# Kernel optimization log

Measured on AMD Instinct MI355X. Metric: run time of the kernel, lower is better.

## Reference

```python
import jax, jax.numpy as jnp
import numpy as np

B = 4096
N_QUBITS = 4
N_LAYERS = 3
C64 = jnp.complex64


def setup_inputs() -> dict:
    key = jax.random.key(0)
    ks = jax.random.split(key, 14)
    f = jax.random.normal
    return {
        "x": f(ks[0], (B, 1, 28, 28), jnp.float32),
        "qparams": f(ks[1], (N_LAYERS, N_QUBITS, 3), jnp.float32),
        "dw4_w": f(ks[2], (4, 1, 4, 4), jnp.float32) * 0.1,
        "dw4_b": f(ks[3], (4,), jnp.float32) * 0.1,
        "pw4_w": f(ks[4], (4, 4, 1, 1), jnp.float32) * 0.3,
        "pw4_b": f(ks[5], (4,), jnp.float32) * 0.1,
        "dw8_w": f(ks[6], (4, 1, 8, 8), jnp.float32) * 0.05,
        "dw8_b": f(ks[7], (4,), jnp.float32) * 0.1,
        "pw8_w": f(ks[8], (4, 4, 1, 1), jnp.float32) * 0.3,
        "pw8_b": f(ks[9], (4,), jnp.float32) * 0.1,
        "res_w": f(ks[10], (4, 1, 1, 1), jnp.float32) * 0.3,
        "res_b": f(ks[11], (4,), jnp.float32) * 0.1,
        "head_w": f(ks[12], (10, 4 * 3 * 14 * 14), jnp.float32) * 0.02,
        "head_b": f(ks[13], (10,), jnp.float32) * 0.02,
    }


def _rx(t):
    c = jnp.cos(t / 2).astype(C64)
    s = (-1j * jnp.sin(t / 2)).astype(C64)
    return jnp.stack([jnp.stack([c, s]), jnp.stack([s, c])])


def _ry(t):
    c = jnp.cos(t / 2)
    s = jnp.sin(t / 2)
    return jnp.stack([jnp.stack([c, -s]), jnp.stack([s, c])]).astype(C64)


def _rz(t):
    z = jnp.zeros((), C64)
    return jnp.stack([jnp.stack([jnp.exp(-0.5j * t).astype(C64), z]),
                      jnp.stack([z, jnp.exp(0.5j * t).astype(C64)])])


def _apply_1q(state, U, wire):
    # state: (n,2,2,2,2); U: (2,2) shared across patches
    st = jnp.moveaxis(state, wire + 1, -1)
    st = jnp.einsum('ij,n...j->n...i', U, st)
    return jnp.moveaxis(st, -1, wire + 1)


def _apply_1q_batched(state, U, wire):
    # U: (n,2,2), one gate per patch (input encoding)
    st = jnp.moveaxis(state, wire + 1, -1)
    st = jnp.einsum('nij,n...j->n...i', U, st)
    return jnp.moveaxis(st, -1, wire + 1)


def _cnot(state, c, t):
    a, b = jnp.split(state, 2, axis=c + 1)
    return jnp.concatenate([a, jnp.flip(b, axis=t + 1)], axis=c + 1)


def _quantum_features(patches, params):
    # patches: (n,4) angles; returns (n,4) PauliZ expectations
    n = patches.shape[0]
    state = jnp.zeros((n, 16), C64).at[:, 0].set(1.0).reshape(n, 2, 2, 2, 2)
    c = jnp.cos(patches / 2)
    s = jnp.sin(patches / 2)
    for q in range(N_QUBITS):
        Uq = jnp.stack([jnp.stack([c[:, q], -s[:, q]], -1),
                        jnp.stack([s[:, q], c[:, q]], -1)], -2).astype(C64)
        state = _apply_1q_batched(state, Uq, q)
    for l in range(N_LAYERS):
        for q in range(N_QUBITS):
            state = _apply_1q(state, _rx(params[l, q, 0]), q)
            state = _apply_1q(state, _ry(params[l, q, 1]), q)
            state = _apply_1q(state, _rz(params[l, q, 2]), q)
        for q in range(N_QUBITS - 1):
            state = _cnot(state, q, q + 1)
        state = _cnot(state, N_QUBITS - 1, 0)
    probs = jnp.real(state * jnp.conj(state))  # (n,2,2,2,2)
    ez = [jnp.sum(jnp.take(probs, 0, axis=q + 1) - jnp.take(probs, 1, axis=q + 1),
                  axis=(1, 2, 3)) for q in range(N_QUBITS)]
    return jnp.stack(ez, -1).astype(jnp.float32)


def _conv(x, w, b, stride):
    y = jax.lax.conv_general_dilated(x, w, (stride, stride), 'VALID',
                                     dimension_numbers=('NCHW', 'OIHW', 'NCHW'))
    return y + b[None, :, None, None]


def _forward(x, qparams, dw4_w, dw4_b, pw4_w, pw4_b, dw8_w, dw8_b, pw8_w, pw8_b,
             res_w, res_b, head_w, head_b):
    b = x.shape[0]
    # residual branch: 1x1 conv then 2x2 avg-pool down to the 14x14 grid
    res = _conv(x, res_w, res_b, 1)                      # (B,4,28,28)
    res = res.reshape(b, 4, 14, 2, 14, 2).mean(axis=(3, 5))  # (B,4,14,14)
    # quantum branch over non-overlapping 2x2 patches
    patches = x[:, 0].reshape(b, 14, 2, 14, 2).transpose(0, 1, 3, 2, 4)
    patches = patches.reshape(b * 14 * 14, 4)
    feat2 = _quantum_features(patches, qparams).reshape(b, 14, 14, 4)
    # multi-scale conv branches, upsampled (nearest) to the 14x14 grid
    feat4 = jax.nn.relu(_conv(_conv(x, dw4_w, dw4_b, 4), pw4_w, pw4_b, 1))  # (B,4,7,7)
    feat4 = jnp.repeat(jnp.repeat(feat4, 2, axis=2), 2, axis=3)             # (B,4,14,14)
    feat8 = jax.nn.relu(_conv(_conv(x, dw8_w, dw8_b, 8), pw8_w, pw8_b, 1))  # (B,4,3,3)
    feat8 = jax.image.resize(feat8, (b, 4, 14, 14), 'nearest')
    f4 = jnp.transpose(feat4, (0, 2, 3, 1))
    f8 = jnp.transpose(feat8, (0, 2, 3, 1))
    r = jnp.transpose(res, (0, 2, 3, 1))
    out = jnp.concatenate([feat2, f4, f8], axis=3) + jnp.tile(r, (1, 1, 1, 3))
    logits = out.reshape(b, -1) @ head_w.T + head_b
    return jax.nn.log_softmax(logits, axis=-1)


def reference(x, qparams, dw4_w, dw4_b, pw4_w, pw4_b, dw8_w, dw8_b, pw8_w, pw8_b,
              res_w, res_b, head_w, head_b):
    return _forward(x, qparams, dw4_w, dw4_b, pw4_w, pw4_b, dw8_w, dw8_b,
                    pw8_w, pw8_b, res_w, res_b, head_w, head_b)
```

## Files before the change

kernel.cpp:

```cpp
#include <hip/hip_runtime.h>

#define WS_T    0
#define WS_HQ   512
#define WS_WA   8352
#define WS_H4   10312
#define WS_H8   12272
#define WS_C10  12632

__device__ __forceinline__ float4 f4fma(const float4 a, const float s, const float4 c) {
  return {fmaf(a.x, s, c.x), fmaf(a.y, s, c.y), fmaf(a.z, s, c.z), fmaf(a.w, s, c.w)};
}
__device__ __forceinline__ float4 f4fma4(const float4 a, const float4 b, const float4 c) {
  return {fmaf(a.x, b.x, c.x), fmaf(a.y, b.y, c.y), fmaf(a.z, b.z, c.z), fmaf(a.w, b.w, c.w)};
}
__device__ __forceinline__ float hsum4(const float4 a) {
  return a.x + a.y + a.z + a.w;
}

__global__ __launch_bounds__(256) void prep_kernel(
    const float* __restrict__ qp, const float* __restrict__ hw,
    const float* __restrict__ res_w, const float* __restrict__ res_b,
    const float* __restrict__ hb, float* __restrict__ ws) {
  __shared__ float row[2352];
  __shared__ float cred[4];
  __shared__ float Sr[16][16];
  __shared__ float Si[16][16];
  __shared__ float csc[36], css[36];
  __shared__ float Afs[256][4];
  const int t = threadIdx.x;

  if (blockIdx.x < 10) {
    const int k = blockIdx.x;
    for (int i = t; i < 2352; i += 256) row[i] = hw[k * 2352 + i];
    __syncthreads();
    float cpart = 0.f;
    if (t < 196) {
      const int b12 = t * 12;
      float4 h = {row[b12], row[b12 + 1], row[b12 + 2], row[b12 + 3]};
      ((float4*)(ws + WS_HQ))[k * 196 + t] = h;
      float wa = 0.f;
#pragma unroll
      for (int c = 0; c < 4; ++c) {
        const float s3 = row[b12 + c] + row[b12 + 4 + c] + row[b12 + 8 + c];
        wa += res_w[c] * s3;
        cpart += res_b[c] * s3;
      }
      ws[WS_WA + k * 196 + t] = wa;
    }
    if (t < 49) {
      const int i4 = t / 7, j4 = t % 7;
      float4 s = {0.f, 0.f, 0.f, 0.f};
#pragma unroll
      for (int di = 0; di < 2; ++di)
#pragma unroll
        for (int dj = 0; dj < 2; ++dj) {
          const int pos = (2 * i4 + di) * 14 + 2 * j4 + dj;
          s.x += row[pos * 12 + 4]; s.y += row[pos * 12 + 5];
          s.z += row[pos * 12 + 6]; s.w += row[pos * 12 + 7];
        }
      ((float4*)(ws + WS_H4))[k * 49 + t] = s;
    }
    if (t < 9) {
      const int i8 = t / 3, j8 = t % 3;
      const int pi0 = (i8 == 0) ? 0 : ((i8 == 1) ? 5 : 9);
      const int pi1 = (i8 == 0) ? 5 : ((i8 == 1) ? 9 : 14);
      const int pj0 = (j8 == 0) ? 0 : ((j8 == 1) ? 5 : 9);
      const int pj1 = (j8 == 0) ? 5 : ((j8 == 1) ? 9 : 14);
      float4 s = {0.f, 0.f, 0.f, 0.f};
      for (int pi = pi0; pi < pi1; ++pi)
        for (int pj = pj0; pj < pj1; ++pj) {
          const int pos = pi * 14 + pj;
          s.x += row[pos * 12 + 8]; s.y += row[pos * 12 + 9];
          s.z += row[pos * 12 + 10]; s.w += row[pos * 12 + 11];
        }
      ((float4*)(ws + WS_H8))[k * 9 + t] = s;
    }
#pragma unroll
    for (int off = 32; off > 0; off >>= 1) cpart += __shfl_xor(cpart, off);
    if ((t & 63) == 0) cred[t >> 6] = cpart;
    __syncthreads();
    if (t == 0) ws[WS_C10 + k] = hb[k] + cred[0] + cred[1] + cred[2] + cred[3];
    return;
  }

  if (t >= 64) return;

  if (t < 36) {
    float th = 0.5f * qp[t];
    csc[t] = cosf(th);
    css[t] = sinf(th);
  }
#pragma unroll
  for (int h = 0; h < 4; ++h) {
    const int idx = t + 64 * h;
    Sr[idx >> 4][idx & 15] = ((idx >> 4) == (idx & 15)) ? 1.f : 0.f;
    Si[idx >> 4][idx & 15] = 0.f;
  }

  for (int l = 0; l < 3; ++l) {
    for (int q = 0; q < 4; ++q) {
      const int m = 8 >> q;
      for (int r = 0; r < 3; ++r) {
        const float c = csc[l * 12 + q * 3 + r];
        const float s = css[l * 12 + q * 3 + r];
#pragma unroll
        for (int h = 0; h < 2; ++h) {
          const int idx = t + 64 * h;
          const int col = idx >> 3, pp = idx & 7;
          const int k = ((pp & ~(m - 1)) << 1) | (pp & (m - 1));
          const int k1 = k | m;
          float a0r = Sr[col][k],  a0i = Si[col][k];
          float a1r = Sr[col][k1], a1i = Si[col][k1];
          float n0r, n0i, n1r, n1i;
          if (r == 0) {
            n0r = c * a0r + s * a1i;  n0i = c * a0i - s * a1r;
            n1r = c * a1r + s * a0i;  n1i = c * a1i - s * a0r;
          } else if (r == 1) {
            n0r = c * a0r - s * a1r;  n0i = c * a0i - s * a1i;
            n1r = s * a0r + c * a1r;  n1i = s * a0i + c * a1i;
          } else {
            n0r = c * a0r + s * a0i;  n0i = c * a0i - s * a0r;
            n1r = c * a1r - s * a1i;  n1i = c * a1i + s * a1r;
          }
          Sr[col][k] = n0r;  Si[col][k] = n0i;
          Sr[col][k1] = n1r; Si[col][k1] = n1i;
        }
      }
    }
    for (int e = 0; e < 4; ++e) {
      const int c2 = t >> 2, p2 = t & 3;
      const int mc = 8 >> e;
      const int mt = 8 >> ((e + 1) & 3);
      const int rest = 15 & ~(mc | mt);
      const int rl = rest & (-rest);
      const int rh = rest ^ rl;
      const int k = mc | ((p2 & 1) ? rl : 0) | ((p2 & 2) ? rh : 0);
      const int k1 = k | mt;
      float tr = Sr[c2][k]; Sr[c2][k] = Sr[c2][k1]; Sr[c2][k1] = tr;
      float ti = Si[c2][k]; Si[c2][k] = Si[c2][k1]; Si[c2][k1] = ti;
    }
  }

#pragma unroll
  for (int h = 0; h < 4; ++h) {
    const int o = t + 64 * h;
    const int i = o >> 4, j = o & 15;
    float a0 = 0.f, a1 = 0.f, a2 = 0.f, a3 = 0.f;
    for (int k = 0; k < 16; ++k) {
      float pr = Sr[i][k] * Sr[j][k] + Si[i][k] * Si[j][k];
      a0 += (k & 8) ? -pr : pr;
      a1 += (k & 4) ? -pr : pr;
      a2 += (k & 2) ? -pr : pr;
      a3 += (k & 1) ? -pr : pr;
    }
    Afs[o][0] = a0; Afs[o][1] = a1; Afs[o][2] = a2; Afs[o][3] = a3;
  }

#pragma unroll
  for (int h = 0; h < 6; ++h) {
    const int o = t + 64 * h;
    if (o < 324) {
      const int mi = o >> 2, q = o & 3;
      const int m0 = mi / 27, m1 = (mi / 9) % 3, m2 = (mi / 3) % 3, m3 = mi % 3;
      const int mm[4] = {m0, m1, m2, m3};
      float acc = 0.f;
      for (int c = 0; c < 16; ++c) {
        int ii = 0, jj = 0; float sg = 1.f;
        for (int qb = 0; qb < 4; ++qb) {
          const int cb = (c >> qb) & 1, bit = 8 >> qb, mq = mm[qb];
          if (mq == 2) { if (cb) ii |= bit; else jj |= bit; }
          else if (cb) { ii |= bit; jj |= bit; if (mq == 1) sg = -sg; }
        }
        acc += sg * Afs[ii * 16 + jj][q];
      }
      ws[WS_T + mi * 4 + q] = acc * 0.0625f;
    }
  }
}

__global__ __launch_bounds__(256, 4) void qmain_kernel(
    const float* __restrict__ x, const float4* __restrict__ T4,
    const float4* __restrict__ HQ4, const float* __restrict__ WA,
    const float4* __restrict__ H44, const float4* __restrict__ H84,
    const float* __restrict__ C10,
    const float* __restrict__ dw4_w, const float* __restrict__ dw4_b,
    const float* __restrict__ pw4_w, const float* __restrict__ pw4_b,
    const float* __restrict__ dw8_w, const float* __restrict__ dw8_b,
    const float* __restrict__ pw8_w, const float* __restrict__ pw8_b,
    float* __restrict__ out, const int B) {
  __shared__ __align__(16) float xs[4 * 792];
  const int t = threadIdx.x;
  const int w = t >> 6, lane = t & 63;
  const int img = blockIdx.x * 4 + w;
  float* xw = xs + w * 792;
  const float4* xw4 = (const float4*)xw;
  const bool ok = (img < B);

  if (ok) {
    const float4* xg = (const float4*)(x + img * 784);
#pragma unroll
    for (int it = 0; it < 4; ++it) {
      const int idx = it * 64 + lane;
      if (idx < 196) ((float4*)xw)[idx] = xg[idx];
    }
  }

  float acc[10];
#pragma unroll
  for (int k = 0; k < 10; ++k) acc[k] = 0.f;

  if (ok && lane < 49) {
    float cc[4][4], ss[4][4], av[4];
#pragma unroll
    for (int s = 0; s < 4; ++s) {
      const int p = 49 * s + lane;
      const int base = 56 * (p / 14) + 2 * (p % 14);
      const float2 a01 = *(const float2*)(xw + base);
      const float2 a23 = *(const float2*)(xw + base + 28);
      __sincosf(a01.x, &ss[s][0], &cc[s][0]);
      __sincosf(a01.y, &ss[s][1], &cc[s][1]);
      __sincosf(a23.x, &ss[s][2], &cc[s][2]);
      __sincosf(a23.y, &ss[s][3], &cc[s][3]);
      av[s] = 0.25f * (a01.x + a01.y + a23.x + a23.y);
    }
    float4 e[4];
#pragma unroll
    for (int s = 0; s < 4; ++s) e[s] = {0.f, 0.f, 0.f, 0.f};
#pragma unroll 1
    for (int g = 0; g < 9; ++g) {
      const float4 t0 = T4[g * 9 + 0], t1 = T4[g * 9 + 1], t2 = T4[g * 9 + 2];
      const float4 t3 = T4[g * 9 + 3], t4 = T4[g * 9 + 4], t5 = T4[g * 9 + 5];
      const float4 t6 = T4[g * 9 + 6], t7 = T4[g * 9 + 7], t8 = T4[g * 9 + 8];
      const int m0 = g / 3, m1 = g % 3;
#pragma unroll
      for (int s = 0; s < 4; ++s) {
        const float c3 = cc[s][3], s3 = ss[s][3];
        const float4 u0 = f4fma(t2, s3, f4fma(t1, c3, t0));
        const float4 u1 = f4fma(t5, s3, f4fma(t4, c3, t3));
        const float4 u2 = f4fma(t8, s3, f4fma(t7, c3, t6));
        const float4 inner = f4fma(u2, ss[s][2], f4fma(u1, cc[s][2], u0));
        const float f0 = (m0 == 0) ? 1.f : ((m0 == 1) ? cc[s][0] : ss[s][0]);
        const float f1 = (m1 == 0) ? 1.f : ((m1 == 1) ? cc[s][1] : ss[s][1]);
        const float wf = (m0 == 0) ? f1 : ((m1 == 0) ? f0 : f0 * f1);
        e[s] = f4fma(inner, wf, e[s]);
      }
    }
#pragma unroll
    for (int k = 0; k < 10; ++k) {
      float a = 0.f;
#pragma unroll
      for (int s = 0; s < 4; ++s) {
        const int p = 49 * s + lane;
        const float4 h = HQ4[k * 196 + p];
        a += fmaf(h.x, e[s].x, fmaf(h.y, e[s].y,
             fmaf(h.z, e[s].z, fmaf(h.w, e[s].w, WA[k * 196 + p] * av[s]))));
      }
      acc[k] = a;
    }
    {
      const int u = lane;
      const int i = u / 7, j = u % 7;
      const float4* w44 = (const float4*)dw4_w;
      float4 q0 = {0.f, 0.f, 0.f, 0.f}, q1 = q0, q2 = q0, q3 = q0;
#pragma unroll
      for (int uu = 0; uu < 4; ++uu) {
        const float4 xa = xw4[(4 * i + uu) * 7 + j];
        q0 = f4fma4(w44[0 + uu], xa, q0);
        q1 = f4fma4(w44[4 + uu], xa, q1);
        q2 = f4fma4(w44[8 + uu], xa, q2);
        q3 = f4fma4(w44[12 + uu], xa, q3);
      }
      const float y0 = hsum4(q0) + dw4_b[0];
      const float y1 = hsum4(q1) + dw4_b[1];
      const float y2 = hsum4(q2) + dw4_b[2];
      const float y3 = hsum4(q3) + dw4_b[3];
      float z[4];
#pragma unroll
      for (int o = 0; o < 4; ++o) {
        float zz = pw4_b[o];
        zz = fmaf(pw4_w[o * 4 + 0], y0, zz);
        zz = fmaf(pw4_w[o * 4 + 1], y1, zz);
        zz = fmaf(pw4_w[o * 4 + 2], y2, zz);
        zz = fmaf(pw4_w[o * 4 + 3], y3, zz);
        z[o] = fmaxf(zz, 0.f);
      }
#pragma unroll
      for (int k = 0; k < 10; ++k) {
        const float4 h = H44[k * 49 + u];
        acc[k] += fmaf(h.x, z[0], fmaf(h.y, z[1], fmaf(h.z, z[2], h.w * z[3])));
      }
    }
  } else if (ok && lane >= 49 && lane < 58) {
    const int pos = lane - 49;
    const int i8 = pos / 3, j8 = pos % 3;
    const float4* w84 = (const float4*)dw8_w;
    float4 e0 = {0.f, 0.f, 0.f, 0.f}, e1 = e0, e2 = e0, e3 = e0;
#pragma unroll
    for (int uu = 0; uu < 8; ++uu) {
      const float4 xa = xw4[(8 * i8 + uu) * 7 + 2 * j8];
      const float4 xb = xw4[(8 * i8 + uu) * 7 + 2 * j8 + 1];
      e0 = f4fma4(w84[0 + uu * 2], xa, e0);
      e0 = f4fma4(w84[1 + uu * 2], xb, e0);
      e1 = f4fma4(w84[16 + uu * 2], xa, e1);
      e1 = f4fma4(w84[17 + uu * 2], xb, e1);
      e2 = f4fma4(w84[32 + uu * 2], xa, e2);
      e2 = f4fma4(w84[33 + uu * 2], xb, e2);
      e3 = f4fma4(w84[48 + uu * 2], xa, e3);
      e3 = f4fma4(w84[49 + uu * 2], xb, e3);
    }
    const float d0 = hsum4(e0) + dw8_b[0];
    const float d1 = hsum4(e1) + dw8_b[1];
    const float d2 = hsum4(e2) + dw8_b[2];
    const float d3 = hsum4(e3) + dw8_b[3];
    float z[4];
#pragma unroll
    for (int o = 0; o < 4; ++o) {
      float zz = pw8_b[o];
      zz = fmaf(pw8_w[o * 4 + 0], d0, zz);
      zz = fmaf(pw8_w[o * 4 + 1], d1, zz);
      zz = fmaf(pw8_w[o * 4 + 2], d2, zz);
      zz = fmaf(pw8_w[o * 4 + 3], d3, zz);
      z[o] = fmaxf(zz, 0.f);
    }
#pragma unroll
    for (int k = 0; k < 10; ++k) {
      const float4 h = H84[k * 9 + pos];
      acc[k] += fmaf(h.x, z[0], fmaf(h.y, z[1], fmaf(h.z, z[2], h.w * z[3])));
    }
  }

  if (!ok) return;

#pragma unroll
  for (int k = 0; k < 10; ++k) {
    float v = acc[k];
    v += __shfl_xor(v, 1);
    v += __shfl_xor(v, 2);
    v += __shfl_xor(v, 4);
    v += __shfl_xor(v, 8);
    v += __shfl_xor(v, 16);
    v += __shfl_xor(v, 32);
    acc[k] = v;
  }

  float lg[10], m = -1e30f;
#pragma unroll
  for (int k = 0; k < 10; ++k) {
    lg[k] = acc[k] + C10[k];
    m = fmaxf(m, lg[k]);
  }
  float se = 0.f;
#pragma unroll
  for (int k = 0; k < 10; ++k) se += __expf(lg[k] - m);
  const float ls = m + __logf(se);
  if (lane < 10) {
    float v = lg[0];
#pragma unroll
    for (int k = 1; k < 10; ++k)
      if (lane == k) v = lg[k];
    out[img * 10 + lane] = v - ls;
  }
}

extern "C" void kernel_launch(void* const* d_in, const int* in_sizes, int n_in,
                              void* d_out, int out_size, void* d_ws, size_t ws_size,
                              hipStream_t stream) {
  const float* x      = (const float*)d_in[0];
  const float* qp     = (const float*)d_in[1];
  const float* dw4_w  = (const float*)d_in[2];
  const float* dw4_b  = (const float*)d_in[3];
  const float* pw4_w  = (const float*)d_in[4];
  const float* pw4_b  = (const float*)d_in[5];
  const float* dw8_w  = (const float*)d_in[6];
  const float* dw8_b  = (const float*)d_in[7];
  const float* pw8_w  = (const float*)d_in[8];
  const float* pw8_b  = (const float*)d_in[9];
  const float* res_w  = (const float*)d_in[10];
  const float* res_b  = (const float*)d_in[11];
  const float* head_w = (const float*)d_in[12];
  const float* head_b = (const float*)d_in[13];
  float* out = (float*)d_out;
  float* ws = (float*)d_ws;
  const int B = in_sizes[0] / 784;

  hipLaunchKernelGGL(prep_kernel, dim3(11), dim3(256), 0, stream,
                     qp, head_w, res_w, res_b, head_b, ws);
  hipLaunchKernelGGL(qmain_kernel, dim3((B + 3) / 4), dim3(256), 0, stream,
                     x, (const float4*)(ws + WS_T),
                     (const float4*)(ws + WS_HQ), ws + WS_WA,
                     (const float4*)(ws + WS_H4), (const float4*)(ws + WS_H8),
                     ws + WS_C10,
                     dw4_w, dw4_b, pw4_w, pw4_b, dw8_w, dw8_b, pw8_w, pw8_b,
                     out, B);
}
```

Before: 33.89 us.

## Split quantum feature evaluation into a separate fully parallel per-patch kernel

Moves the per-patch quantum expectation computation out of the main kernel, where only 49 of 64 lanes worked on 4 patches each, into a new kernel with one thread per patch across all images. The results (4 expectations plus the patch average) go to a global workspace and the main kernel reads them back. This raises parallelism and removes lane idling for the trig-heavy part, at the cost of an extra launch and a round trip through global memory of about 16 MB. It also fuses the three rotation gates per qubit in the prep kernel into one pass over shared memory.

```diff
diff --git a/kernel.cpp b/kernel.cpp
--- a/kernel.cpp
+++ b/kernel.cpp
@@ -6,6 +6,8 @@
 #define WS_H4   10312
 #define WS_H8   12272
 #define WS_C10  12632
+#define WS_E4   262144
+#define WS_AV   3473408
 
 __device__ __forceinline__ float4 f4fma(const float4 a, const float s, const float4 c) {
   return {fmaf(a.x, s, c.x), fmaf(a.y, s, c.y), fmaf(a.z, s, c.z), fmaf(a.w, s, c.w)};
@@ -100,31 +102,25 @@
   for (int l = 0; l < 3; ++l) {
     for (int q = 0; q < 4; ++q) {
       const int m = 8 >> q;
-      for (int r = 0; r < 3; ++r) {
-        const float c = csc[l * 12 + q * 3 + r];
-        const float s = css[l * 12 + q * 3 + r];
-#pragma unroll
-        for (int h = 0; h < 2; ++h) {
-          const int idx = t + 64 * h;
-          const int col = idx >> 3, pp = idx & 7;
-          const int k = ((pp & ~(m - 1)) << 1) | (pp & (m - 1));
-          const int k1 = k | m;
-          float a0r = Sr[col][k],  a0i = Si[col][k];
-          float a1r = Sr[col][k1], a1i = Si[col][k1];
-          float n0r, n0i, n1r, n1i;
-          if (r == 0) {
-            n0r = c * a0r + s * a1i;  n0i = c * a0i - s * a1r;
-            n1r = c * a1r + s * a0i;  n1i = c * a1i - s * a0r;
-          } else if (r == 1) {
-            n0r = c * a0r - s * a1r;  n0i = c * a0i - s * a1i;
-            n1r = s * a0r + c * a1r;  n1i = s * a0i + c * a1i;
-          } else {
-            n0r = c * a0r + s * a0i;  n0i = c * a0i - s * a0r;
-            n1r = c * a1r - s * a1i;  n1i = c * a1i + s * a1r;
-          }
-          Sr[col][k] = n0r;  Si[col][k] = n0i;
-          Sr[col][k1] = n1r; Si[col][k1] = n1i;
-        }
+      const float cx = csc[l * 12 + q * 3 + 0], sx = css[l * 12 + q * 3 + 0];
+      const float cy = csc[l * 12 + q * 3 + 1], sy = css[l * 12 + q * 3 + 1];
+      const float cz = csc[l * 12 + q * 3 + 2], sz = css[l * 12 + q * 3 + 2];
+#pragma unroll
+      for (int h = 0; h < 2; ++h) {
+        const int idx = t + 64 * h;
+        const int col = idx >> 3, pp = idx & 7;
+        const int k = ((pp & ~(m - 1)) << 1) | (pp & (m - 1));
+        const int k1 = k | m;
+        float a0r = Sr[col][k],  a0i = Si[col][k];
+        float a1r = Sr[col][k1], a1i = Si[col][k1];
+        const float x0r = cx * a0r + sx * a1i, x0i = cx * a0i - sx * a1r;
+        const float x1r = cx * a1r + sx * a0i, x1i = cx * a1i - sx * a0r;
+        const float y0r = cy * x0r - sy * x1r, y0i = cy * x0i - sy * x1i;
+        const float y1r = sy * x0r + cy * x1r, y1i = sy * x0i + cy * x1i;
+        a0r = cz * y0r + sz * y0i;  a0i = cz * y0i - sz * y0r;
+        a1r = cz * y1r - sz * y1i;  a1i = cz * y1i + sz * y1r;
+        Sr[col][k] = a0r;  Si[col][k] = a0i;
+        Sr[col][k1] = a1r; Si[col][k1] = a1i;
       }
     }
     for (int e = 0; e < 4; ++e) {
@@ -178,8 +174,41 @@
   }
 }
 
+__global__ __launch_bounds__(256) void qfeat_kernel(
+    const float* __restrict__ x, const float4* __restrict__ T4,
+    float4* __restrict__ e4out, float* __restrict__ avout, const int NP) {
+  const int gp = blockIdx.x * 256 + threadIdx.x;
+  if (gp >= NP) return;
+  const int img = gp / 196, p = gp - img * 196;
+  const int pi = p / 14, pj = p - pi * 14;
+  const float* xb = x + img * 784 + 56 * pi + 2 * pj;
+  const float2 a01 = *(const float2*)(xb);
+  const float2 a23 = *(const float2*)(xb + 28);
+  float c0, s0, c1, s1, c2, s2, c3, s3;
+  __sincosf(a01.x, &s0, &c0);
+  __sincosf(a01.y, &s1, &c1);
+  __sincosf(a23.x, &s2, &c2);
+  __sincosf(a23.y, &s3, &c3);
+  const float w01[9] = {1.f, c1, s1, c0, c0 * c1, c0 * s1, s0, s0 * c1, s0 * s1};
+  float4 e = {0.f, 0.f, 0.f, 0.f};
+#pragma unroll
+  for (int g = 0; g < 9; ++g) {
+    const float4 t0 = T4[g * 9 + 0], t1 = T4[g * 9 + 1], t2 = T4[g * 9 + 2];
+    const float4 t3 = T4[g * 9 + 3], t4 = T4[g * 9 + 4], t5 = T4[g * 9 + 5];
+    const float4 t6 = T4[g * 9 + 6], t7 = T4[g * 9 + 7], t8 = T4[g * 9 + 8];
+    const float4 u0 = f4fma(t2, s3, f4fma(t1, c3, t0));
+    const float4 u1 = f4fma(t5, s3, f4fma(t4, c3, t3));
+    const float4 u2 = f4fma(t8, s3, f4fma(t7, c3, t6));
+    const float4 inner = f4fma(u2, s2, f4fma(u1, c2, u0));
+    e = f4fma(inner, w01[g], e);
+  }
+  e4out[gp] = e;
+  avout[gp] = 0.25f * (a01.x + a01.y + a23.x + a23.y);
+}
+
 __global__ __launch_bounds__(256, 4) void qmain_kernel(
-    const float* __restrict__ x, const float4* __restrict__ T4,
+    const float* __restrict__ x, const float4* __restrict__ E4,
+    const float* __restrict__ AV,
     const float4* __restrict__ HQ4, const float* __restrict__ WA,
     const float4* __restrict__ H44, const float4* __restrict__ H84,
     const float* __restrict__ C10,
@@ -210,40 +239,13 @@
   for (int k = 0; k < 10; ++k) acc[k] = 0.f;
 
   if (ok && lane < 49) {
-    float cc[4][4], ss[4][4], av[4];
+    float4 e[4];
+    float av[4];
 #pragma unroll
     for (int s = 0; s < 4; ++s) {
-      const int p = 49 * s + lane;
-      const int base = 56 * (p / 14) + 2 * (p % 14);
-      const float2 a01 = *(const float2*)(xw + base);
-      const float2 a23 = *(const float2*)(xw + base + 28);
-      __sincosf(a01.x, &ss[s][0], &cc[s][0]);
-      __sincosf(a01.y, &ss[s][1], &cc[s][1]);
-      __sincosf(a23.x, &ss[s][2], &cc[s][2]);
-      __sincosf(a23.y, &ss[s][3], &cc[s][3]);
-      av[s] = 0.25f * (a01.x + a01.y + a23.x + a23.y);
-    }
-    float4 e[4];
-#pragma unroll
-    for (int s = 0; s < 4; ++s) e[s] = {0.f, 0.f, 0.f, 0.f};
-#pragma unroll 1
-    for (int g = 0; g < 9; ++g) {
-      const float4 t0 = T4[g * 9 + 0], t1 = T4[g * 9 + 1], t2 = T4[g * 9 + 2];
-      const float4 t3 = T4[g * 9 + 3], t4 = T4[g * 9 + 4], t5 = T4[g * 9 + 5];
-      const float4 t6 = T4[g * 9 + 6], t7 = T4[g * 9 + 7], t8 = T4[g * 9 + 8];
-      const int m0 = g / 3, m1 = g % 3;
-#pragma unroll
-      for (int s = 0; s < 4; ++s) {
-        const float c3 = cc[s][3], s3 = ss[s][3];
-        const float4 u0 = f4fma(t2, s3, f4fma(t1, c3, t0));
-        const float4 u1 = f4fma(t5, s3, f4fma(t4, c3, t3));
-        const float4 u2 = f4fma(t8, s3, f4fma(t7, c3, t6));
-        const float4 inner = f4fma(u2, ss[s][2], f4fma(u1, cc[s][2], u0));
-        const float f0 = (m0 == 0) ? 1.f : ((m0 == 1) ? cc[s][0] : ss[s][0]);
-        const float f1 = (m1 == 0) ? 1.f : ((m1 == 1) ? cc[s][1] : ss[s][1]);
-        const float wf = (m0 == 0) ? f1 : ((m1 == 0) ? f0 : f0 * f1);
-        e[s] = f4fma(inner, wf, e[s]);
-      }
+      const int gp = img * 196 + 49 * s + lane;
+      e[s] = E4[gp];
+      av[s] = AV[gp];
     }
 #pragma unroll
     for (int k = 0; k < 10; ++k) {
@@ -382,11 +384,15 @@
   float* out = (float*)d_out;
   float* ws = (float*)d_ws;
   const int B = in_sizes[0] / 784;
+  const int NP = B * 196;
 
   hipLaunchKernelGGL(prep_kernel, dim3(11), dim3(256), 0, stream,
                      qp, head_w, res_w, res_b, head_b, ws);
+  hipLaunchKernelGGL(qfeat_kernel, dim3((NP + 255) / 256), dim3(256), 0, stream,
+                     x, (const float4*)(ws + WS_T),
+                     (float4*)(ws + WS_E4), ws + WS_AV, NP);
   hipLaunchKernelGGL(qmain_kernel, dim3((B + 3) / 4), dim3(256), 0, stream,
-                     x, (const float4*)(ws + WS_T),
+                     x, (const float4*)(ws + WS_E4), ws + WS_AV,
                      (const float4*)(ws + WS_HQ), ws + WS_WA,
                      (const float4*)(ws + WS_H4), (const float4*)(ws + WS_H8),
                      ws + WS_C10,
```

Result: slower. 42.55 us (+25.6%).
